# Optimization experiments

Hardware: AMD Instinct MI355X
Metric: run time of the kernel (lower is better)

## Reference

```python
import jax, jax.numpy as jnp
import numpy as np


def setup_inputs() -> dict:
    key = jax.random.key(0)
    k1, k2 = jax.random.split(key)
    B, N = 2, 8192
    pred = jax.random.normal(k1, (B, N, 3), dtype=jnp.float32)
    gt = jax.random.normal(k2, (B, N, 3), dtype=jnp.float32)
    return {"pred": pred, "gt": gt}


def reference(pred, gt):
    # dist[b, i, j] = ||pred[b, j] - gt[b, i]||_2, computed via the
    # squared-norm expansion to avoid materializing a [B,N,N,3] diff tensor.
    p_sq = jnp.sum(pred * pred, axis=-1)  # [B, N]
    g_sq = jnp.sum(gt * gt, axis=-1)      # [B, N]
    # inner[b, i, j] = gt[b, i] . pred[b, j]
    inner = jnp.einsum("bid,bjd->bij", gt, pred)  # [B, N, N]
    sq_dist = g_sq[:, :, None] + p_sq[:, None, :] - 2.0 * inner
    dist = jnp.sqrt(jnp.maximum(sq_dist, 0.0))    # [B, N, N]
    dist1 = jnp.min(dist, axis=2)  # per-gt nearest pred distance, [B, N]
    dist2 = jnp.min(dist, axis=1)  # per-pred nearest gt distance, [B, N]
    chamfer = (dist1.mean(axis=1) + dist2.mean(axis=1)).mean()
    return chamfer
```

## Files before the change

### kernel.cpp

```cpp
#include <hip/hip_runtime.h>
#include <math.h>

#define NPTS  8192
#define BATCH 2
#define CJ    256
#define IPT   4
#define TPB   256
#define NSLOT (2 * BATCH * NPTS)
#define GX    (NSLOT / (TPB * IPT))
#define GY    (NPTS / CJ)

typedef float v2f __attribute__((ext_vector_type(2)));
typedef float v4f __attribute__((ext_vector_type(4)));

__global__ __launch_bounds__(TPB) void chamfer_pairs(
    const float* __restrict__ pred, const float* __restrict__ gt,
    unsigned int* __restrict__ mins)
{
    __shared__ v4f xs4[CJ / 4], ys4[CJ / 4], zs4[CJ / 4], qs4[CJ / 4];

    const int base  = blockIdx.x * (TPB * IPT);
    const int dir   = base >> 14;
    const int b     = (base >> 13) & 1;
    const int ibase = base & (NPTS - 1);

    const float* pts  = (dir == 0 ? gt : pred) + (size_t)b * NPTS * 3;
    const float* cand = (dir == 0 ? pred : gt) + (size_t)b * NPTS * 3;

    const int j0 = blockIdx.y * CJ;
    {
        float* xs = (float*)xs4; float* ys = (float*)ys4;
        float* zs = (float*)zs4; float* qs = (float*)qs4;
        for (int jj = threadIdx.x; jj < CJ; jj += TPB) {
            float x = cand[(size_t)(j0 + jj) * 3 + 0];
            float y = cand[(size_t)(j0 + jj) * 3 + 1];
            float z = cand[(size_t)(j0 + jj) * 3 + 2];
            xs[jj] = x; ys[jj] = y; zs[jj] = z;
            qs[jj] = 0.5f * (x * x + y * y + z * z);
        }
    }

    float px[IPT], py[IPT], pz[IPT], m[IPT];
#pragma unroll
    for (int k = 0; k < IPT; ++k) {
        int i = ibase + threadIdx.x + k * TPB;
        px[k] = pts[(size_t)i * 3 + 0];
        py[k] = pts[(size_t)i * 3 + 1];
        pz[k] = pts[(size_t)i * 3 + 2];
        m[k]  = 3.0e38f;
    }
    __syncthreads();

#pragma unroll 4
    for (int j = 0; j < CJ / 4; ++j) {
        v4f cx = xs4[j], cy = ys4[j], cz = zs4[j], cq = qs4[j];
        v2f cxa = cx.xy, cxb = cx.zw, cya = cy.xy, cyb = cy.zw;
        v2f cza = cz.xy, czb = cz.zw, cqa = cq.xy, cqb = cq.zw;
#pragma unroll
        for (int k = 0; k < IPT; ++k) {
            v2f ta = cqa - cxa * px[k];
            ta = ta - cya * py[k];
            ta = ta - cza * pz[k];
            v2f tb = cqb - cxb * px[k];
            tb = tb - cyb * py[k];
            tb = tb - czb * pz[k];
            m[k] = fminf(fminf(m[k], ta.x), ta.y);
            m[k] = fminf(fminf(m[k], tb.x), tb.y);
        }
    }

#pragma unroll
    for (int k = 0; k < IPT; ++k) {
        float gsq = fmaf(px[k], px[k], fmaf(py[k], py[k], pz[k] * pz[k]));
        float d2  = fmaxf(fmaf(2.0f, m[k], gsq), 0.0f);
        atomicMin(&mins[base + k * TPB + threadIdx.x], __float_as_uint(d2));
    }
}

__global__ __launch_bounds__(1024) void chamfer_reduce(
    const unsigned int* __restrict__ mins, float* __restrict__ out)
{
    float s = 0.f;
#pragma unroll
    for (int r = 0; r < NSLOT / 1024; ++r)
        s += sqrtf(__uint_as_float(mins[r * 1024 + threadIdx.x]));

    for (int off = 32; off > 0; off >>= 1)
        s += __shfl_down(s, off, 64);

    __shared__ float ws[16];
    const int wave = threadIdx.x >> 6, lane = threadIdx.x & 63;
    if (lane == 0) ws[wave] = s;
    __syncthreads();
    if (threadIdx.x == 0) {
        float t = 0.f;
#pragma unroll
        for (int w = 0; w < 16; ++w) t += ws[w];
        out[0] = t * (1.0f / (float)(BATCH * NPTS));
    }
}

extern "C" void kernel_launch(void* const* d_in, const int* in_sizes, int n_in,
                              void* d_out, int out_size, void* d_ws, size_t ws_size,
                              hipStream_t stream) {
    const float* pred = (const float*)d_in[0];
    const float* gt   = (const float*)d_in[1];
    unsigned int* mins = (unsigned int*)d_ws;

    dim3 grid(GX, GY);
    chamfer_pairs<<<grid, TPB, 0, stream>>>(pred, gt, mins);
    chamfer_reduce<<<1, 1024, 0, stream>>>(mins, (float*)d_out);
}
```

Baseline: 79.63 us.

## Replace global atomicMin with per-tile partial minima and parallel reduce

Each tile block now writes its per-point squared minima to a private row of a partial buffer instead of doing atomicMin into a shared slot array. A multi-block reduce kernel takes the min across rows, applies sqrt, sums, and atomically accumulates into a zeroed output. Tile shape also changes to fewer candidates per block and more points per thread. This removes atomic contention and the single-block reduce, at the cost of a large intermediate buffer with extra global traffic plus a memset launch, and higher register use.

```diff
diff --git a/kernel.cpp b/kernel.cpp
--- a/kernel.cpp
+++ b/kernel.cpp
@@ -3,19 +3,19 @@
 
 #define NPTS  8192
 #define BATCH 2
-#define CJ    256
-#define IPT   4
+#define GY    64
+#define CJ    (NPTS / GY)
+#define IPT   8
 #define TPB   256
 #define NSLOT (2 * BATCH * NPTS)
 #define GX    (NSLOT / (TPB * IPT))
-#define GY    (NPTS / CJ)
 
 typedef float v2f __attribute__((ext_vector_type(2)));
 typedef float v4f __attribute__((ext_vector_type(4)));
 
 __global__ __launch_bounds__(TPB) void chamfer_pairs(
     const float* __restrict__ pred, const float* __restrict__ gt,
-    unsigned int* __restrict__ mins)
+    float* __restrict__ part)
 {
     __shared__ v4f xs4[CJ / 4], ys4[CJ / 4], zs4[CJ / 4], qs4[CJ / 4];
 
@@ -28,16 +28,13 @@
     const float* cand = (dir == 0 ? pred : gt) + (size_t)b * NPTS * 3;
 
     const int j0 = blockIdx.y * CJ;
-    {
-        float* xs = (float*)xs4; float* ys = (float*)ys4;
-        float* zs = (float*)zs4; float* qs = (float*)qs4;
-        for (int jj = threadIdx.x; jj < CJ; jj += TPB) {
-            float x = cand[(size_t)(j0 + jj) * 3 + 0];
-            float y = cand[(size_t)(j0 + jj) * 3 + 1];
-            float z = cand[(size_t)(j0 + jj) * 3 + 2];
-            xs[jj] = x; ys[jj] = y; zs[jj] = z;
-            qs[jj] = 0.5f * (x * x + y * y + z * z);
-        }
+    if (threadIdx.x < CJ) {
+        int jj = threadIdx.x;
+        float x = cand[(size_t)(j0 + jj) * 3 + 0];
+        float y = cand[(size_t)(j0 + jj) * 3 + 1];
+        float z = cand[(size_t)(j0 + jj) * 3 + 2];
+        ((float*)xs4)[jj] = x; ((float*)ys4)[jj] = y; ((float*)zs4)[jj] = z;
+        ((float*)qs4)[jj] = 0.5f * (x * x + y * y + z * z);
     }
 
     float px[IPT], py[IPT], pz[IPT], m[IPT];
@@ -69,34 +66,35 @@
         }
     }
 
+    float* prow = part + (size_t)blockIdx.y * NSLOT + base;
 #pragma unroll
     for (int k = 0; k < IPT; ++k) {
         float gsq = fmaf(px[k], px[k], fmaf(py[k], py[k], pz[k] * pz[k]));
         float d2  = fmaxf(fmaf(2.0f, m[k], gsq), 0.0f);
-        atomicMin(&mins[base + k * TPB + threadIdx.x], __float_as_uint(d2));
+        prow[k * TPB + threadIdx.x] = d2;
     }
 }
 
-__global__ __launch_bounds__(1024) void chamfer_reduce(
-    const unsigned int* __restrict__ mins, float* __restrict__ out)
+__global__ __launch_bounds__(TPB) void chamfer_reduce(
+    const float* __restrict__ part, float* __restrict__ out)
 {
-    float s = 0.f;
-#pragma unroll
-    for (int r = 0; r < NSLOT / 1024; ++r)
-        s += sqrtf(__uint_as_float(mins[r * 1024 + threadIdx.x]));
+    const int s = blockIdx.x * TPB + threadIdx.x;
+    float m = part[s];
+#pragma unroll 8
+    for (int g = 1; g < GY; ++g)
+        m = fminf(m, part[(size_t)g * NSLOT + s]);
 
+    float v = sqrtf(m);
     for (int off = 32; off > 0; off >>= 1)
-        s += __shfl_down(s, off, 64);
+        v += __shfl_down(v, off, 64);
 
-    __shared__ float ws[16];
+    __shared__ float ws[TPB / 64];
     const int wave = threadIdx.x >> 6, lane = threadIdx.x & 63;
-    if (lane == 0) ws[wave] = s;
+    if (lane == 0) ws[wave] = v;
     __syncthreads();
     if (threadIdx.x == 0) {
-        float t = 0.f;
-#pragma unroll
-        for (int w = 0; w < 16; ++w) t += ws[w];
-        out[0] = t * (1.0f / (float)(BATCH * NPTS));
+        float t = (ws[0] + ws[1]) + (ws[2] + ws[3]);
+        atomicAdd(out, t * (1.0f / (float)(BATCH * NPTS)));
     }
 }
 
@@ -105,9 +103,11 @@
                               hipStream_t stream) {
     const float* pred = (const float*)d_in[0];
     const float* gt   = (const float*)d_in[1];
-    unsigned int* mins = (unsigned int*)d_ws;
+    float* part = (float*)d_ws;
+
+    hipMemsetAsync(d_out, 0, sizeof(float), stream);
 
     dim3 grid(GX, GY);
-    chamfer_pairs<<<grid, TPB, 0, stream>>>(pred, gt, mins);
-    chamfer_reduce<<<1, 1024, 0, stream>>>(mins, (float*)d_out);
+    chamfer_pairs<<<grid, TPB, 0, stream>>>(pred, gt, part);
+    chamfer_reduce<<<NSLOT / TPB, TPB, 0, stream>>>(part, (float*)d_out);
 }
```

After: 88.94 us. 1.12x slower.

## Replace atomicMin scatter with per-chunk partial buffer and parallel min-reduce

Applied to the files above, without the earlier changes.

Instead of each pair block doing atomicMin into a shared mins array, each block writes its partial minima to its own row of a [GY, NSLOT] buffer. A multi-block reduce kernel takes the min across rows, applies sqrt, sums, and atomically adds into the output, which is zeroed by a memset. The candidate chunk size is set from GY=32, so CJ stays 256. This removes atomic contention and the single-block reduce, at the cost of writing and reading a 4 MB partial buffer and an extra memset launch.

```diff
diff --git a/kernel.cpp b/kernel.cpp
--- a/kernel.cpp
+++ b/kernel.cpp
@@ -3,19 +3,19 @@
 
 #define NPTS  8192
 #define BATCH 2
-#define CJ    256
+#define GY    32
+#define CJ    (NPTS / GY)
 #define IPT   4
 #define TPB   256
 #define NSLOT (2 * BATCH * NPTS)
 #define GX    (NSLOT / (TPB * IPT))
-#define GY    (NPTS / CJ)
 
 typedef float v2f __attribute__((ext_vector_type(2)));
 typedef float v4f __attribute__((ext_vector_type(4)));
 
 __global__ __launch_bounds__(TPB) void chamfer_pairs(
     const float* __restrict__ pred, const float* __restrict__ gt,
-    unsigned int* __restrict__ mins)
+    float* __restrict__ part)
 {
     __shared__ v4f xs4[CJ / 4], ys4[CJ / 4], zs4[CJ / 4], qs4[CJ / 4];
 
@@ -69,35 +69,38 @@
         }
     }
 
+    float* prow = part + (size_t)blockIdx.y * NSLOT + base;
 #pragma unroll
     for (int k = 0; k < IPT; ++k) {
         float gsq = fmaf(px[k], px[k], fmaf(py[k], py[k], pz[k] * pz[k]));
         float d2  = fmaxf(fmaf(2.0f, m[k], gsq), 0.0f);
-        atomicMin(&mins[base + k * TPB + threadIdx.x], __float_as_uint(d2));
+        prow[k * TPB + threadIdx.x] = d2;
     }
 }
 
-__global__ __launch_bounds__(1024) void chamfer_reduce(
-    const unsigned int* __restrict__ mins, float* __restrict__ out)
+__global__ __launch_bounds__(128) void chamfer_reduce(
+    const float* __restrict__ part, float* __restrict__ out)
 {
-    float s = 0.f;
+    const int s = blockIdx.x * 128 + threadIdx.x;
+    float v[GY];
 #pragma unroll
-    for (int r = 0; r < NSLOT / 1024; ++r)
-        s += sqrtf(__uint_as_float(mins[r * 1024 + threadIdx.x]));
+    for (int g = 0; g < GY; ++g)
+        v[g] = part[(size_t)g * NSLOT + s];
 
+    float m = v[0];
+#pragma unroll
+    for (int g = 1; g < GY; ++g) m = fminf(m, v[g]);
+
+    float sum = sqrtf(m);
     for (int off = 32; off > 0; off >>= 1)
-        s += __shfl_down(s, off, 64);
+        sum += __shfl_down(sum, off, 64);
 
-    __shared__ float ws[16];
+    __shared__ float ws[2];
     const int wave = threadIdx.x >> 6, lane = threadIdx.x & 63;
-    if (lane == 0) ws[wave] = s;
+    if (lane == 0) ws[wave] = sum;
     __syncthreads();
-    if (threadIdx.x == 0) {
-        float t = 0.f;
-#pragma unroll
-        for (int w = 0; w < 16; ++w) t += ws[w];
-        out[0] = t * (1.0f / (float)(BATCH * NPTS));
-    }
+    if (threadIdx.x == 0)
+        atomicAdd(out, (ws[0] + ws[1]) * (1.0f / (float)(BATCH * NPTS)));
 }
 
 extern "C" void kernel_launch(void* const* d_in, const int* in_sizes, int n_in,
@@ -105,9 +108,11 @@
                               hipStream_t stream) {
     const float* pred = (const float*)d_in[0];
     const float* gt   = (const float*)d_in[1];
-    unsigned int* mins = (unsigned int*)d_ws;
+    float* part = (float*)d_ws;
+
+    hipMemsetAsync(d_out, 0, sizeof(float), stream);
 
     dim3 grid(GX, GY);
-    chamfer_pairs<<<grid, TPB, 0, stream>>>(pred, gt, mins);
-    chamfer_reduce<<<1, 1024, 0, stream>>>(mins, (float*)d_out);
+    chamfer_pairs<<<grid, TPB, 0, stream>>>(pred, gt, part);
+    chamfer_reduce<<<NSLOT / 128, 128, 0, stream>>>(part, (float*)d_out);
 }
```

Result: slower. 81.34 us (+2.2%).
